# Kernel tuning notes

Measured on AMD Instinct MI355X. Metric: run time of the kernel, lower is better.

## Reference

```python
import jax, jax.numpy as jnp
import numpy as np
from jax.scipy.special import logsumexp

EPSILON = 0.1
MAX_ITERS = 20

B, S, T = 8, 2048, 2048


def setup_inputs() -> dict:
    key = jax.random.key(0)
    k1, k2, k3 = jax.random.split(key, 3)
    cost = jax.random.normal(k1, (B, S, T), dtype=jnp.float32)
    mu = jax.random.uniform(k2, (B, S), dtype=jnp.float32)
    nu = jax.random.uniform(k3, (B, T), dtype=jnp.float32)
    # normalize to probability distributions (realistic OT marginals)
    mu = mu / jnp.sum(mu, axis=-1, keepdims=True)
    nu = nu / jnp.sum(nu, axis=-1, keepdims=True)
    return {"cost": cost, "mu": mu, "nu": nu}


def reference(cost, mu, nu):
    tiny = jnp.finfo(cost.dtype).tiny
    log_mu = jnp.log(jnp.maximum(mu, tiny))          # (B, S)
    log_nu = jnp.log(jnp.maximum(nu, tiny))          # (B, T)
    log_K = -cost / EPSILON                          # (B, S, T)

    def step(carry, _):
        log_u, log_v = carry
        # row update: logsumexp over targets
        log_u = log_mu - logsumexp(log_K + log_v[:, None, :], axis=-1)  # (B, S)
        # col update: logsumexp over sources (equiv. to transpose in torch code)
        log_v = log_nu - logsumexp(log_K + log_u[:, :, None], axis=-2)  # (B, T)
        return (log_u, log_v), None

    init = (jnp.zeros_like(log_mu), jnp.zeros_like(log_nu))
    (log_u, log_v), _ = jax.lax.scan(step, init, None, length=MAX_ITERS)

    log_pi = log_u[:, :, None] + log_K + log_v[:, None, :]  # (B, S, T)
    transport = jnp.exp(log_pi)
    return transport, log_pi
```

## Files before the change

### kernel.cpp

```cpp
#include <hip/hip_runtime.h>
#include <hip/hip_fp16.h>
#include <math.h>

#define BB 8
#define SS 2048
#define TT 2048
#define ITERS 20
#define NEG_EPS_INV -10.0f
#define RPW 2
#define NWAVE 4
#define ROWS (RPW * NWAVE)
#define NTILE (SS / ROWS)
#define TINYF 1.17549435e-38f

__device__ __forceinline__ float4 fma4v(float a, float4 x, float4 y) {
    return make_float4(fmaf(a, x.x, y.x), fmaf(a, x.y, y.y),
                       fmaf(a, x.z, y.z), fmaf(a, x.w, y.w));
}
__device__ __forceinline__ float4 max4(float4 a, float4 b) {
    return make_float4(fmaxf(a.x, b.x), fmaxf(a.y, b.y),
                       fmaxf(a.z, b.z), fmaxf(a.w, b.w));
}
__device__ __forceinline__ float hmax4(float4 a) {
    return fmaxf(fmaxf(a.x, a.y), fmaxf(a.z, a.w));
}
__device__ __forceinline__ float hsum4(float4 a) {
    return (a.x + a.y) + (a.z + a.w);
}
__device__ __forceinline__ float4 exp4m(float4 x, float m) {
    return make_float4(__expf(x.x - m), __expf(x.y - m),
                       __expf(x.z - m), __expf(x.w - m));
}
__device__ __forceinline__ uint h2u(__half2 h) {
    union { __half2 h; uint u; } c; c.h = h; return c.u;
}
__device__ __forceinline__ __half2 u2h(uint u) {
    union { __half2 h; uint u; } c; c.u = u; return c.h;
}
__device__ __forceinline__ uint2 pack4(float4 f) {
    uint2 r;
    r.x = h2u(__float22half2_rn(make_float2(f.x, f.y)));
    r.y = h2u(__float22half2_rn(make_float2(f.z, f.w)));
    return r;
}
__device__ __forceinline__ float4 unpack4(uint2 u) {
    float2 a = __half22float2(u2h(u.x));
    float2 b = __half22float2(u2h(u.y));
    return make_float4(a.x, a.y, b.x, b.y);
}

__global__ __launch_bounds__(256) void init_logv(float* __restrict__ log_v) {
    log_v[blockIdx.x * 256 + threadIdx.x] = 0.0f;
}

template <bool FIRST>
__global__ __launch_bounds__(256, 3) void fused_pass(
        const float* __restrict__ cost, const uint2* __restrict__ c16r,
        uint2* __restrict__ c16w, const float* __restrict__ mu,
        const float* __restrict__ log_v, float* __restrict__ log_u,
        float* __restrict__ P) {
    int t = threadIdx.x;
    int w = t >> 6, l = t & 63;
    int tile = blockIdx.x, b = blockIdx.y;
    int r0 = tile * ROWS + w * RPW;

    size_t rowbase = (size_t)(b * SS + r0) * TT;
    const float4* v4 = (const float4*)(log_v + (size_t)b * TT);

    float4 vv[8];
#pragma unroll
    for (int i = 0; i < 8; ++i) vv[i] = v4[i * 64 + l];

    float4 x0[8], x1[8];
    if constexpr (FIRST) {
        const float4* c4 = (const float4*)(cost + rowbase);
        uint2* cw = c16w + rowbase / 4;
#pragma unroll
        for (int i = 0; i < 8; ++i) x0[i] = c4[i * 64 + l];
#pragma unroll
        for (int i = 0; i < 8; ++i) x1[i] = c4[512 + i * 64 + l];
#pragma unroll
        for (int i = 0; i < 8; ++i) {
            cw[i * 64 + l] = pack4(x0[i]);
            cw[512 + i * 64 + l] = pack4(x1[i]);
        }
    } else {
        const uint2* cr = c16r + rowbase / 4;
#pragma unroll
        for (int i = 0; i < 8; ++i) x0[i] = unpack4(cr[i * 64 + l]);
#pragma unroll
        for (int i = 0; i < 8; ++i) x1[i] = unpack4(cr[512 + i * 64 + l]);
    }
#pragma unroll
    for (int i = 0; i < 8; ++i) {
        x0[i] = fma4v(NEG_EPS_INV, x0[i], vv[i]);
        x1[i] = fma4v(NEG_EPS_INV, x1[i], vv[i]);
    }

    float4 a0 = x0[0], a1 = x1[0];
#pragma unroll
    for (int i = 1; i < 8; ++i) { a0 = max4(a0, x0[i]); a1 = max4(a1, x1[i]); }
    float m0 = hmax4(a0), m1 = hmax4(a1);
#pragma unroll
    for (int off = 1; off < 64; off <<= 1) {
        m0 = fmaxf(m0, __shfl_xor(m0, off));
        m1 = fmaxf(m1, __shfl_xor(m1, off));
    }

    float ps0 = 0.0f, ps1 = 0.0f;
#pragma unroll
    for (int i = 0; i < 8; ++i) {
        x0[i] = exp4m(x0[i], m0);
        x1[i] = exp4m(x1[i], m1);
        ps0 += hsum4(x0[i]);
        ps1 += hsum4(x1[i]);
    }
#pragma unroll
    for (int off = 1; off < 64; off <<= 1) {
        ps0 += __shfl_xor(ps0, off);
        ps1 += __shfl_xor(ps1, off);
    }

    float g0 = mu[b * SS + r0] / ps0;
    float g1 = mu[b * SS + r0 + 1] / ps1;
    if (l == 0) {
        log_u[b * SS + r0]     = __logf(fmaxf(g0, TINYF)) - m0;
        log_u[b * SS + r0 + 1] = __logf(fmaxf(g1, TINYF)) - m1;
    }

    __shared__ float4 lds[NWAVE][512];
#pragma unroll
    for (int i = 0; i < 8; ++i) {
        float4 cs;
        cs.x = fmaf(g0, x0[i].x, g1 * x1[i].x);
        cs.y = fmaf(g0, x0[i].y, g1 * x1[i].y);
        cs.z = fmaf(g0, x0[i].z, g1 * x1[i].z);
        cs.w = fmaf(g0, x0[i].w, g1 * x1[i].w);
        lds[w][i * 64 + l] = cs;
    }
    __syncthreads();

    float4* P4 = (float4*)P + (size_t)(tile * BB + b) * 512;
#pragma unroll
    for (int k = 0; k < 2; ++k) {
        int j = k * 256 + t;
        float4 s0 = lds[0][j], s1 = lds[1][j], s2 = lds[2][j], s3 = lds[3][j];
        float4 o;
        o.x = (s0.x + s1.x) + (s2.x + s3.x);
        o.y = (s0.y + s1.y) + (s2.y + s3.y);
        o.z = (s0.z + s1.z) + (s2.z + s3.z);
        o.w = (s0.w + s1.w) + (s2.w + s3.w);
        P4[j] = o;
    }
}

__global__ __launch_bounds__(256) void combine_v(
        const float* __restrict__ P, const float* __restrict__ nu,
        float* __restrict__ log_v) {
    int t = threadIdx.x;
    int seg = t >> 6, ci = t & 63;
    int col = blockIdx.x * 64 + ci;
    int b = blockIdx.y;

    float s = 0.0f;
#pragma unroll 8
    for (int k = 0; k < NTILE / 4; ++k) {
        int tile = seg * (NTILE / 4) + k;
        s += P[((size_t)tile * BB + b) * TT + col];
    }
    __shared__ float lds[4][64];
    lds[seg][ci] = s;
    __syncthreads();
    if (t < 64) {
        float tot = (lds[0][ci] + lds[1][ci]) + (lds[2][ci] + lds[3][ci]);
        int i = b * TT + col;
        log_v[i] = __logf(fmaxf(nu[i], TINYF)) + log_v[i] - __logf(fmaxf(tot, TINYF));
    }
}

__global__ __launch_bounds__(256) void finalize(const float* __restrict__ cost,
                                                const float* __restrict__ log_u,
                                                const float* __restrict__ log_v,
                                                float* __restrict__ transport,
                                                float* __restrict__ log_pi) {
    int i = blockIdx.x * 256 + threadIdx.x;
    int flat = i * 4;
    int row = flat >> 11;
    int t = flat & (TT - 1);
    int b = row >> 11;

    float lu = log_u[row];
    float4 lv = *reinterpret_cast<const float4*>(log_v + (size_t)b * TT + t);
    float4 c = *reinterpret_cast<const float4*>(cost + (size_t)row * TT + t);

    float4 lp;
    lp.x = fmaf(NEG_EPS_INV, c.x, lu + lv.x);
    lp.y = fmaf(NEG_EPS_INV, c.y, lu + lv.y);
    lp.z = fmaf(NEG_EPS_INV, c.z, lu + lv.z);
    lp.w = fmaf(NEG_EPS_INV, c.w, lu + lv.w);

    float4 tr;
    tr.x = __expf(lp.x);
    tr.y = __expf(lp.y);
    tr.z = __expf(lp.z);
    tr.w = __expf(lp.w);

    *reinterpret_cast<float4*>(transport + (size_t)row * TT + t) = tr;
    *reinterpret_cast<float4*>(log_pi + (size_t)row * TT + t) = lp;
}

extern "C" void kernel_launch(void* const* d_in, const int* in_sizes, int n_in,
                              void* d_out, int out_size, void* d_ws, size_t ws_size,
                              hipStream_t stream) {
    const float* cost = (const float*)d_in[0];
    const float* mu = (const float*)d_in[1];
    const float* nu = (const float*)d_in[2];

    float* out = (float*)d_out;
    float* transport = out;
    float* log_pi = out + (size_t)BB * SS * TT;

    float* ws = (float*)d_ws;
    float* log_u = ws;
    float* log_v = ws + 16384;
    float* P = ws + (1 << 20);
    uint2* c16 = (uint2*)(ws + (1 << 23));

    hipLaunchKernelGGL(init_logv, dim3(BB * TT / 256), dim3(256), 0, stream, log_v);

    hipLaunchKernelGGL((fused_pass<true>), dim3(NTILE, BB), dim3(256), 0, stream,
                       cost, c16, c16, mu, log_v, log_u, P);
    hipLaunchKernelGGL(combine_v, dim3(TT / 64, BB), dim3(256), 0, stream,
                       P, nu, log_v);

    for (int it = 1; it < ITERS; ++it) {
        hipLaunchKernelGGL((fused_pass<false>), dim3(NTILE, BB), dim3(256), 0, stream,
                           cost, c16, c16, mu, log_v, log_u, P);
        hipLaunchKernelGGL(combine_v, dim3(TT / 64, BB), dim3(256), 0, stream,
                           P, nu, log_v);
    }

    hipLaunchKernelGGL(finalize, dim3(BB * SS * TT / 4 / 256), dim3(256), 0, stream,
                       cost, log_u, log_v, transport, log_pi);
}
```

Baseline: 508.1 us.

## Accumulate four row chunks per block and read fp16 cost in finalize

Each fused_pass block now processes 32 rows in four chunks and accumulates the column partial sums in registers. This cuts the partial-sum buffer, and the combine_v reads of it, by a factor of four, but launches fewer blocks. finalize reads the cached fp16 cost copy instead of fp32 cost, which halves its input traffic but adds fp16 rounding error to log_pi. It also writes outputs with nontemporal stores to avoid polluting the cache.

```diff
diff --git a/kernel.cpp b/kernel.cpp
--- a/kernel.cpp
+++ b/kernel.cpp
@@ -7,11 +7,12 @@
 #define TT 2048
 #define ITERS 20
 #define NEG_EPS_INV -10.0f
-#define RPW 2
-#define NWAVE 4
-#define ROWS (RPW * NWAVE)
+#define ROWS 32
+#define NCHUNK 4
 #define NTILE (SS / ROWS)
 #define TINYF 1.17549435e-38f
+
+typedef float vfloat4 __attribute__((ext_vector_type(4)));
 
 __device__ __forceinline__ float4 fma4v(float a, float4 x, float4 y) {
     return make_float4(fmaf(a, x.x, y.x), fmaf(a, x.y, y.y),
@@ -47,6 +48,10 @@
     float2 a = __half22float2(u2h(u.x));
     float2 b = __half22float2(u2h(u.y));
     return make_float4(a.x, a.y, b.x, b.y);
+}
+__device__ __forceinline__ void nt_store4(float4 v, float* p) {
+    vfloat4 x = {v.x, v.y, v.z, v.w};
+    __builtin_nontemporal_store(x, reinterpret_cast<vfloat4*>(p));
 }
 
 __global__ __launch_bounds__(256) void init_logv(float* __restrict__ log_v) {
@@ -62,82 +67,90 @@
     int t = threadIdx.x;
     int w = t >> 6, l = t & 63;
     int tile = blockIdx.x, b = blockIdx.y;
-    int r0 = tile * ROWS + w * RPW;
-
-    size_t rowbase = (size_t)(b * SS + r0) * TT;
+
     const float4* v4 = (const float4*)(log_v + (size_t)b * TT);
-
     float4 vv[8];
 #pragma unroll
     for (int i = 0; i < 8; ++i) vv[i] = v4[i * 64 + l];
 
-    float4 x0[8], x1[8];
-    if constexpr (FIRST) {
-        const float4* c4 = (const float4*)(cost + rowbase);
-        uint2* cw = c16w + rowbase / 4;
-#pragma unroll
-        for (int i = 0; i < 8; ++i) x0[i] = c4[i * 64 + l];
-#pragma unroll
-        for (int i = 0; i < 8; ++i) x1[i] = c4[512 + i * 64 + l];
+    float4 acc[8];
+#pragma unroll
+    for (int i = 0; i < 8; ++i) acc[i] = make_float4(0.f, 0.f, 0.f, 0.f);
+
+#pragma unroll
+    for (int c = 0; c < NCHUNK; ++c) {
+        int r0 = tile * ROWS + c * 8 + w * 2;
+        size_t rowbase = (size_t)(b * SS + r0) * TT;
+
+        float4 x0[8], x1[8];
+        if constexpr (FIRST) {
+            const float4* c4 = (const float4*)(cost + rowbase);
+            uint2* cw = c16w + rowbase / 4;
+#pragma unroll
+            for (int i = 0; i < 8; ++i) x0[i] = c4[i * 64 + l];
+#pragma unroll
+            for (int i = 0; i < 8; ++i) x1[i] = c4[512 + i * 64 + l];
+#pragma unroll
+            for (int i = 0; i < 8; ++i) {
+                cw[i * 64 + l] = pack4(x0[i]);
+                cw[512 + i * 64 + l] = pack4(x1[i]);
+            }
+        } else {
+            const uint2* cr = c16r + rowbase / 4;
+#pragma unroll
+            for (int i = 0; i < 8; ++i) x0[i] = unpack4(cr[i * 64 + l]);
+#pragma unroll
+            for (int i = 0; i < 8; ++i) x1[i] = unpack4(cr[512 + i * 64 + l]);
+        }
 #pragma unroll
         for (int i = 0; i < 8; ++i) {
-            cw[i * 64 + l] = pack4(x0[i]);
-            cw[512 + i * 64 + l] = pack4(x1[i]);
-        }
-    } else {
-        const uint2* cr = c16r + rowbase / 4;
-#pragma unroll
-        for (int i = 0; i < 8; ++i) x0[i] = unpack4(cr[i * 64 + l]);
-#pragma unroll
-        for (int i = 0; i < 8; ++i) x1[i] = unpack4(cr[512 + i * 64 + l]);
-    }
-#pragma unroll
-    for (int i = 0; i < 8; ++i) {
-        x0[i] = fma4v(NEG_EPS_INV, x0[i], vv[i]);
-        x1[i] = fma4v(NEG_EPS_INV, x1[i], vv[i]);
-    }
-
-    float4 a0 = x0[0], a1 = x1[0];
-#pragma unroll
-    for (int i = 1; i < 8; ++i) { a0 = max4(a0, x0[i]); a1 = max4(a1, x1[i]); }
-    float m0 = hmax4(a0), m1 = hmax4(a1);
-#pragma unroll
-    for (int off = 1; off < 64; off <<= 1) {
-        m0 = fmaxf(m0, __shfl_xor(m0, off));
-        m1 = fmaxf(m1, __shfl_xor(m1, off));
-    }
-
-    float ps0 = 0.0f, ps1 = 0.0f;
-#pragma unroll
-    for (int i = 0; i < 8; ++i) {
-        x0[i] = exp4m(x0[i], m0);
-        x1[i] = exp4m(x1[i], m1);
-        ps0 += hsum4(x0[i]);
-        ps1 += hsum4(x1[i]);
-    }
-#pragma unroll
-    for (int off = 1; off < 64; off <<= 1) {
-        ps0 += __shfl_xor(ps0, off);
-        ps1 += __shfl_xor(ps1, off);
-    }
-
-    float g0 = mu[b * SS + r0] / ps0;
-    float g1 = mu[b * SS + r0 + 1] / ps1;
-    if (l == 0) {
-        log_u[b * SS + r0]     = __logf(fmaxf(g0, TINYF)) - m0;
-        log_u[b * SS + r0 + 1] = __logf(fmaxf(g1, TINYF)) - m1;
-    }
-
-    __shared__ float4 lds[NWAVE][512];
-#pragma unroll
-    for (int i = 0; i < 8; ++i) {
-        float4 cs;
-        cs.x = fmaf(g0, x0[i].x, g1 * x1[i].x);
-        cs.y = fmaf(g0, x0[i].y, g1 * x1[i].y);
-        cs.z = fmaf(g0, x0[i].z, g1 * x1[i].z);
-        cs.w = fmaf(g0, x0[i].w, g1 * x1[i].w);
-        lds[w][i * 64 + l] = cs;
-    }
+            x0[i] = fma4v(NEG_EPS_INV, x0[i], vv[i]);
+            x1[i] = fma4v(NEG_EPS_INV, x1[i], vv[i]);
+        }
+
+        float4 a0 = x0[0], a1 = x1[0];
+#pragma unroll
+        for (int i = 1; i < 8; ++i) { a0 = max4(a0, x0[i]); a1 = max4(a1, x1[i]); }
+        float m0 = hmax4(a0), m1 = hmax4(a1);
+#pragma unroll
+        for (int off = 1; off < 64; off <<= 1) {
+            m0 = fmaxf(m0, __shfl_xor(m0, off));
+            m1 = fmaxf(m1, __shfl_xor(m1, off));
+        }
+
+        float ps0 = 0.0f, ps1 = 0.0f;
+#pragma unroll
+        for (int i = 0; i < 8; ++i) {
+            x0[i] = exp4m(x0[i], m0);
+            x1[i] = exp4m(x1[i], m1);
+            ps0 += hsum4(x0[i]);
+            ps1 += hsum4(x1[i]);
+        }
+#pragma unroll
+        for (int off = 1; off < 64; off <<= 1) {
+            ps0 += __shfl_xor(ps0, off);
+            ps1 += __shfl_xor(ps1, off);
+        }
+
+        float g0 = mu[b * SS + r0] / ps0;
+        float g1 = mu[b * SS + r0 + 1] / ps1;
+        if (l == 0) {
+            log_u[b * SS + r0]     = __logf(fmaxf(g0, TINYF)) - m0;
+            log_u[b * SS + r0 + 1] = __logf(fmaxf(g1, TINYF)) - m1;
+        }
+
+#pragma unroll
+        for (int i = 0; i < 8; ++i) {
+            acc[i].x = fmaf(g0, x0[i].x, fmaf(g1, x1[i].x, acc[i].x));
+            acc[i].y = fmaf(g0, x0[i].y, fmaf(g1, x1[i].y, acc[i].y));
+            acc[i].z = fmaf(g0, x0[i].z, fmaf(g1, x1[i].z, acc[i].z));
+            acc[i].w = fmaf(g0, x0[i].w, fmaf(g1, x1[i].w, acc[i].w));
+        }
+    }
+
+    __shared__ float4 lds[4][512];
+#pragma unroll
+    for (int i = 0; i < 8; ++i) lds[w][i * 64 + l] = acc[i];
     __syncthreads();
 
     float4* P4 = (float4*)P + (size_t)(tile * BB + b) * 512;
@@ -163,7 +176,7 @@
     int b = blockIdx.y;
 
     float s = 0.0f;
-#pragma unroll 8
+#pragma unroll 4
     for (int k = 0; k < NTILE / 4; ++k) {
         int tile = seg * (NTILE / 4) + k;
         s += P[((size_t)tile * BB + b) * TT + col];
@@ -178,7 +191,7 @@
     }
 }
 
-__global__ __launch_bounds__(256) void finalize(const float* __restrict__ cost,
+__global__ __launch_bounds__(256) void finalize(const uint2* __restrict__ c16,
                                                 const float* __restrict__ log_u,
                                                 const float* __restrict__ log_v,
                                                 float* __restrict__ transport,
@@ -191,7 +204,7 @@
 
     float lu = log_u[row];
     float4 lv = *reinterpret_cast<const float4*>(log_v + (size_t)b * TT + t);
-    float4 c = *reinterpret_cast<const float4*>(cost + (size_t)row * TT + t);
+    float4 c = unpack4(c16[((size_t)row * TT + t) / 4]);
 
     float4 lp;
     lp.x = fmaf(NEG_EPS_INV, c.x, lu + lv.x);
@@ -205,8 +218,8 @@
     tr.z = __expf(lp.z);
     tr.w = __expf(lp.w);
 
-    *reinterpret_cast<float4*>(transport + (size_t)row * TT + t) = tr;
-    *reinterpret_cast<float4*>(log_pi + (size_t)row * TT + t) = lp;
+    nt_store4(tr, transport + (size_t)row * TT + t);
+    nt_store4(lp, log_pi + (size_t)row * TT + t);
 }
 
 extern "C" void kernel_launch(void* const* d_in, const int* in_sizes, int n_in,
@@ -241,5 +254,5 @@
     }
 
     hipLaunchKernelGGL(finalize, dim3(BB * SS * TT / 4 / 256), dim3(256), 0, stream,
-                       cost, log_u, log_v, transport, log_pi);
-}
+                       c16, log_u, log_v, transport, log_pi);
+}
```

After: 946.4 us. +86.3%, slower.
